# Performance work log

Measured on AMD Instinct MI355X. Metric: run time of the kernel, lower is better.

## Reference

```python
import jax, jax.numpy as jnp
import numpy as np

GRID_SIZE = 5
SPLINE_ORDER = 3
NUM_BASIS = GRID_SIZE + SPLINE_ORDER  # 8


def make_grid():
    # knots: grid_size + 2*spline_order + 1 = 12 points over extended [-1,1]
    h = 2.0 / GRID_SIZE
    return (jnp.arange(-SPLINE_ORDER, GRID_SIZE + SPLINE_ORDER + 1, dtype=jnp.float32) * h - 1.0)[None, :]  # (1, 12)


def b_splines(x, grid):
    # x: (N, in) -> bases: (N, in, NUM_BASIS) via Cox-de Boor recursion
    x = x[..., None]  # (N, in, 1)
    bases = ((x >= grid[:, :-1]) & (x < grid[:, 1:])).astype(x.dtype)
    for p in range(1, SPLINE_ORDER + 1):
        left = (x - grid[:, : -(p + 1)]) / (grid[:, p:-1] - grid[:, : -(p + 1)])
        right = (grid[:, p + 1:] - x) / (grid[:, p + 1:] - grid[:, 1:-p])
        bases = left * bases[..., :-1] + right * bases[..., 1:]
    return bases


def kan_linear(x, base_w, spline_w, scaler, grid):
    # x: (N, in); base_w: (out, in); spline_w: (out, in, G); scaler: (out, in)
    base = jnp.einsum('ni,oi->no', jax.nn.silu(x), base_w)
    bases = b_splines(x, grid)  # (N, in, G)
    spline = jnp.einsum('nig,oig->no', bases, spline_w * scaler[..., None])
    return base + spline


def setup_inputs() -> dict:
    key = jax.random.key(0)
    ks = jax.random.split(key, 7)
    H, L = 768, 2
    hidden = jax.random.normal(ks[0], (32, 512, H), dtype=jnp.float32)
    s = 0.1
    return {
        'hidden': hidden,
        'base_w1': jax.random.normal(ks[1], (H, H), jnp.float32) * s,
        'spline_w1': jax.random.normal(ks[2], (H, H, NUM_BASIS), jnp.float32) * s,
        'scaler1': jax.random.normal(ks[3], (H, H), jnp.float32) * s + 1.0,
        'base_w2': jax.random.normal(ks[4], (L, H), jnp.float32) * s,
        'spline_w2': jax.random.normal(ks[5], (L, H, NUM_BASIS), jnp.float32) * s,
        'scaler2': jax.random.normal(ks[6], (L, H), jnp.float32) * s + 1.0,
    }


def reference(hidden, base_w1, spline_w1, scaler1, base_w2, spline_w2, scaler2):
    grid = make_grid()
    B, S, H = hidden.shape
    x = hidden.reshape(-1, H)  # (N, H)
    x = kan_linear(x, base_w1, spline_w1, scaler1, grid)
    x = jax.nn.gelu(x, approximate=False)  # torch F.gelu default = erf
    out = kan_linear(x, base_w2, spline_w2, scaler2, grid)  # (N, L)
    return out.reshape(B, S, -1).squeeze(-1) if out.shape[-1] == 1 else out.reshape(B, S, -1)
```

## Files before the change

### kernel.cpp

```cpp
#include <hip/hip_runtime.h>
#include <math.h>

#define NROWS 16384
#define H     768
#define KEXP  6912
#define NCHUNK 108
#define NITER 54

typedef __attribute__((ext_vector_type(8))) short  bhalf8;
typedef __attribute__((ext_vector_type(4))) float  floatx4;

__device__ __forceinline__ unsigned short f2bf(float f) {
    unsigned int u = __float_as_uint(f);
    u = (u + 0x7FFFu + ((u >> 16) & 1u)) >> 16;
    return (unsigned short)u;
}
__device__ __forceinline__ float bf2f(unsigned short h) {
    return __uint_as_float(((unsigned int)h) << 16);
}
__device__ __forceinline__ unsigned int pack2(unsigned short a, unsigned short b) {
    return (unsigned int)a | ((unsigned int)b << 16);
}
__device__ __forceinline__ float silu_f(float x) { return x / (1.0f + __expf(-x)); }

__device__ __forceinline__ float gelu_fast(float x) {
    float x3 = x * x * x;
    float y = fmaf(x3, 0.0356774081f, x * 0.7978845608f);
    float e = __expf(2.0f * y);
    float th = 1.0f - 2.0f / (e + 1.0f);
    return 0.5f * x * (1.0f + th);
}

__device__ __forceinline__ void kan_bases(float x, float* __restrict__ b) {
    const float c6 = 0.166666666667f;
    float u  = fmaf(x, 2.5f, 5.5f);
    float fj = floorf(u);
    float t  = u - fj;
    int  j0  = (int)fj;
    float t2 = t * t, t3 = t2 * t;
    float n0 = t3 * c6;
    float n1 = fmaf(t3, -0.5f, fmaf(t2, 0.5f, fmaf(t, 0.5f, c6)));
    float n2 = fmaf(t3, 0.5f, fmaf(t2, -1.0f, 0.666666666667f));
    float omt = 1.0f - t;
    float n3 = omt * omt * omt * c6;
#pragma unroll
    for (int c = 0; c < 8; ++c) {
        int d = j0 - c;
        float v = (d == 0) ? n0 : 0.0f;
        v = (d == 1) ? n1 : v;
        v = (d == 2) ? n2 : v;
        v = (d == 3) ? n3 : v;
        b[c] = v;
    }
}

__global__ __launch_bounds__(256) void prep_expand(
    const float* __restrict__ x, const float* __restrict__ bw,
    const float* __restrict__ sw, const float* __restrict__ sc,
    unsigned short* __restrict__ wp, unsigned short* __restrict__ F)
{
    const int b = blockIdx.x, t = threadIdx.x;
    if (b < 6144) {
        const int e0 = b * 2048 + t;
#pragma unroll
        for (int j = 0; j < 8; ++j) {
            int e = e0 + j * 256;
            int n = e / 768;
            int i = e - n * 768;
            float xv = x[e];
            unsigned short* out = F + (size_t)n * KEXP;
            out[i] = f2bf(silu_f(xv));
            float bb[8];
            kan_bases(xv, bb);
            uint4 pk;
            pk.x = pack2(f2bf(bb[0]), f2bf(bb[1]));
            pk.y = pack2(f2bf(bb[2]), f2bf(bb[3]));
            pk.z = pack2(f2bf(bb[4]), f2bf(bb[5]));
            pk.w = pack2(f2bf(bb[6]), f2bf(bb[7]));
            *(uint4*)(out + H + (size_t)i * 8) = pk;
        }
    } else {
        const int n = b - 6144;
        const float* bwr = bw + (size_t)n * H;
        unsigned short* out = wp + (size_t)n * KEXP;
        if (t < 96) {
            const float4* xp = (const float4*)(bwr + t * 8);
            float4 v0 = xp[0], v1 = xp[1];
            uint4 pk;
            pk.x = pack2(f2bf(v0.x), f2bf(v0.y));
            pk.y = pack2(f2bf(v0.z), f2bf(v0.w));
            pk.z = pack2(f2bf(v1.x), f2bf(v1.y));
            pk.w = pack2(f2bf(v1.z), f2bf(v1.w));
            *(uint4*)(out + t * 8) = pk;
        }
#pragma unroll
        for (int p = 0; p < 3; ++p) {
            int i = t + p * 256;
            float s = sc[(size_t)n * H + i];
            const float4* swp = (const float4*)(sw + ((size_t)n * H + i) * 8);
            float4 w0 = swp[0], w1 = swp[1];
            uint4 pk;
            pk.x = pack2(f2bf(w0.x * s), f2bf(w0.y * s));
            pk.y = pack2(f2bf(w0.z * s), f2bf(w0.w * s));
            pk.z = pack2(f2bf(w1.x * s), f2bf(w1.y * s));
            pk.w = pack2(f2bf(w1.z * s), f2bf(w1.w * s));
            *(uint4*)(out + H + (size_t)i * 8) = pk;
        }
    }
}


#define AS1 __attribute__((address_space(1)))
#define AS3 __attribute__((address_space(3)))

#define DSR(D, A, O) asm volatile("ds_read_b128 %0, %1 offset:" #O : "=v"(D) : "v"(A) : "memory")
#define LDA0(O) do{ DSR(fA0[0],avA[0],O); DSR(fA0[1],avA[1],O); DSR(fA0[2],avA[2],O); DSR(fA0[3],avA[3],O); \
                    DSR(fA0[4],avA[4],O); DSR(fA0[5],avA[5],O); DSR(fA0[6],avA[6],O); DSR(fA0[7],avA[7],O); }while(0)
#define LDA1(O) do{ DSR(fA1[0],avA[0],O); DSR(fA1[1],avA[1],O); DSR(fA1[2],avA[2],O); DSR(fA1[3],avA[3],O); \
                    DSR(fA1[4],avA[4],O); DSR(fA1[5],avA[5],O); DSR(fA1[6],avA[6],O); DSR(fA1[7],avA[7],O); }while(0)
#define LDB(O)  do{ DSR(fB[0],avB[0],O); DSR(fB[1],avB[1],O); }while(0)

#define MM0(QN) do{ \
    _Pragma("unroll") \
    for (int kk = 0; kk < 2; ++kk) \
        _Pragma("unroll") \
        for (int im = 0; im < 4; ++im) \
            acc0[QN][im] = __builtin_amdgcn_mfma_f32_16x16x32_bf16( \
                fA0[im*2+kk], fB[kk], acc0[QN][im], 0, 0, 0); \
}while(0)
#define MM1(QN) do{ \
    _Pragma("unroll") \
    for (int kk = 0; kk < 2; ++kk) \
        _Pragma("unroll") \
        for (int im = 0; im < 4; ++im) \
            acc1[QN][im] = __builtin_amdgcn_mfma_f32_16x16x32_bf16( \
                fA1[im*2+kk], fB[kk], acc1[QN][im], 0, 0, 0); \
}while(0)

#define STG_A(BF,HH,KS) do{ \
    __builtin_amdgcn_global_load_lds((const AS1 void*)(pA##HH[0] + (size_t)(KS)*64), \
        (AS3 void*)&sA[BF][HH][wb8], 16, 0, 0); \
    __builtin_amdgcn_global_load_lds((const AS1 void*)(pA##HH[1] + (size_t)(KS)*64), \
        (AS3 void*)&sA[BF][HH][4096 + wb8], 16, 0, 0); \
}while(0)
#define STG_B(BF,QN,KS) \
    __builtin_amdgcn_global_load_lds((const AS1 void*)(pB[QN] + (size_t)(KS)*64), \
        (AS3 void*)&sB[BF][QN][wb8], 16, 0, 0)

#define PH_MID do{ __builtin_amdgcn_s_barrier(); \
    asm volatile("s_waitcnt lgkmcnt(0)" ::: "memory"); \
    __builtin_amdgcn_sched_barrier(0); \
    __builtin_amdgcn_s_setprio(1); }while(0)
#define PH_END do{ __builtin_amdgcn_s_setprio(0); \
    __builtin_amdgcn_sched_barrier(0); \
    __builtin_amdgcn_s_barrier(); }while(0)
#define PH_END_VMN(N) do{ __builtin_amdgcn_s_setprio(0); \
    __builtin_amdgcn_sched_barrier(0); \
    asm volatile("s_waitcnt vmcnt(" #N ")" ::: "memory"); \
    __builtin_amdgcn_s_barrier(); }while(0)

#define EPI_HALF(ACC, QMOFF) do{ \
    _Pragma("unroll") \
    for (int im = 0; im < 4; ++im) { \
        _Pragma("unroll") \
        for (int rg = 0; rg < 4; ++rg) { \
            float p0 = 0.f, p1 = 0.f; \
            _Pragma("unroll") \
            for (int qn = 0; qn < 3; ++qn) { \
                float v = ACC[qn][im][rg]; \
                float u = gelu_fast(v); \
                float f0v = silu_f(u); \
                float bb[8]; \
                kan_bases(u, bb); \
                float t0 = bb[0]*wsw[qn][0][0].x + bb[1]*wsw[qn][0][0].y \
                         + bb[2]*wsw[qn][0][0].z + bb[3]*wsw[qn][0][0].w \
                         + bb[4]*wsw[qn][0][1].x + bb[5]*wsw[qn][0][1].y \
                         + bb[6]*wsw[qn][0][1].z + bb[7]*wsw[qn][0][1].w; \
                float t1 = bb[0]*wsw[qn][1][0].x + bb[1]*wsw[qn][1][0].y \
                         + bb[2]*wsw[qn][1][0].z + bb[3]*wsw[qn][1][0].w \
                         + bb[4]*wsw[qn][1][1].x + bb[5]*wsw[qn][1][1].y \
                         + bb[6]*wsw[qn][1][1].z + bb[7]*wsw[qn][1][1].w; \
                p0 += fmaf(f0v, wbw[qn][0], wsc[qn][0] * t0); \
                p1 += fmaf(f0v, wbw[qn][1], wsc[qn][1] * t1); \
            } \
            _Pragma("unroll") \
            for (int off = 8; off > 0; off >>= 1) { \
                p0 += __shfl_xor(p0, off, 64); \
                p1 += __shfl_xor(p1, off, 64); \
            } \
            if (lm == 0) { \
                int row = rowBase + (QMOFF) + wr*64 + im*16 + quad*4 + rg; \
                atomicAdd(&outp[(size_t)row * 2 + 0], p0); \
                atomicAdd(&outp[(size_t)row * 2 + 1], p1); \
            } \
        } \
    } \
}while(0)

__global__ __launch_bounds__(512, 2) void kan1_fused(
    const unsigned short* __restrict__ F, const unsigned short* __restrict__ wp,
    const float* __restrict__ bw2, const float* __restrict__ sw2,
    const float* __restrict__ sc2, float* __restrict__ outp)
{
    __shared__ __align__(16) unsigned short sA[2][2][8192];
    __shared__ __align__(16) unsigned short sB[2][3][4096];

    const int b = blockIdx.x;
    const int s = b >> 3;
    const int rowT = (b & 7) * 8 + (s >> 2);
    const int colT = s & 3;
    const int rowBase = rowT * 256, colBase = colT * 192;

    const int t = threadIdx.x;
    const int lane = t & 63;
    const int quad = lane >> 4, lm = lane & 15, p7 = lane & 7;
    const int wv = t >> 6, wr = wv & 1, wc = wv >> 1;

    const int rr = t >> 3;
    const int slotx = (t & 7) ^ (rr & 7);
    const int wb8 = (t & 448) * 8;

    const unsigned short* pA0[2]; const unsigned short* pA1[2];
    const unsigned short* pB[3];
#pragma unroll
    for (int p = 0; p < 2; ++p) {
        pA0[p] = F + (size_t)(rowBase +       p*64 + rr) * KEXP + slotx*8;
        pA1[p] = F + (size_t)(rowBase + 128 + p*64 + rr) * KEXP + slotx*8;
    }
#pragma unroll
    for (int q = 0; q < 3; ++q)
        pB[q] = wp + (size_t)(colBase + q*64 + rr) * KEXP + slotx*8;

    unsigned int avA[8], avB[2];
    {
        unsigned int aB = (unsigned int)(size_t)(AS3 unsigned short*)&sA[0][0][0];
        unsigned int bB = (unsigned int)(size_t)(AS3 unsigned short*)&sB[0][0][0];
#pragma unroll
        for (int im = 0; im < 4; ++im)
#pragma unroll
            for (int kk = 0; kk < 2; ++kk)
                avA[im*2+kk] = aB + (unsigned)(((wr*64 + im*16 + lm)*64 + (((kk*4+quad)^p7)*8)) * 2);
#pragma unroll
        for (int kk = 0; kk < 2; ++kk)
            avB[kk] = bB + (unsigned)(((wc*16 + lm)*64 + (((kk*4+quad)^p7)*8)) * 2);
    }

    floatx4 acc0[3][4] = {};
    floatx4 acc1[3][4] = {};
    bhalf8 fA0[8], fA1[8], fB[2];

    STG_A(0,0,0); STG_A(0,1,0); STG_B(0,0,0); STG_B(0,1,0); STG_B(0,2,0);
    STG_A(1,0,1); STG_A(1,1,1); STG_B(1,0,1); STG_B(1,1,1);
    asm volatile("s_waitcnt vmcnt(8)" ::: "memory");
    __builtin_amdgcn_s_barrier();

#pragma unroll 1
    for (int i = 0; i < NITER; ++i) {
        const int k1 = 2*i + 1;
        const int k2 = (2*i + 2 > 107) ? 107 : 2*i + 2;
        const int k3 = (2*i + 3 > 107) ? 107 : 2*i + 3;
        LDA0(0);     LDB(0);     STG_B(1,2,k1);               PH_MID; MM0(0);         PH_END_VMN(10);
        LDA1(16384);             STG_A(0,0,k2);               PH_MID; MM1(0);         PH_END_VMN(10);
        LDB(8192);               STG_A(0,1,k2);               PH_MID; MM1(1); MM0(1); PH_END_VMN(11);
        LDB(16384);              STG_B(0,0,k2); STG_B(0,1,k2);PH_MID; MM0(2); MM1(2); PH_END_VMN(8);
        LDA0(32768); LDB(24576); STG_B(0,2,k2);               PH_MID; MM0(0);         PH_END;
        LDA1(49152);             STG_A(1,0,k3);               PH_MID; MM1(0);         PH_END_VMN(10);
        LDB(32768);              STG_A(1,1,k3);               PH_MID; MM1(1); MM0(1); PH_END_VMN(11);
        LDB(40960);              STG_B(1,0,k3); STG_B(1,1,k3);PH_MID; MM0(2); MM1(2); PH_END_VMN(8);
    }

    float  wbw[3][2], wsc[3][2];
    float4 wsw[3][2][2];
#pragma unroll
    for (int qn = 0; qn < 3; ++qn) {
        const int i = colBase + qn*64 + wc*16 + lm;
        wbw[qn][0] = bw2[i];      wbw[qn][1] = bw2[H + i];
        wsc[qn][0] = sc2[i];      wsc[qn][1] = sc2[H + i];
        const float4* q0 = (const float4*)(sw2 + (size_t)i * 8);
        const float4* q1 = (const float4*)(sw2 + (size_t)(H + i) * 8);
        wsw[qn][0][0] = q0[0];    wsw[qn][0][1] = q0[1];
        wsw[qn][1][0] = q1[0];    wsw[qn][1][1] = q1[1];
    }
    EPI_HALF(acc0, 0);
    EPI_HALF(acc1, 128);
}

extern "C" void kernel_launch(void* const* d_in, const int* in_sizes, int n_in,
                              void* d_out, int out_size, void* d_ws, size_t ws_size,
                              hipStream_t stream) {
    const float* hidden = (const float*)d_in[0];
    const float* bw1    = (const float*)d_in[1];
    const float* sw1    = (const float*)d_in[2];
    const float* sc1    = (const float*)d_in[3];
    const float* bw2    = (const float*)d_in[4];
    const float* sw2    = (const float*)d_in[5];
    const float* sc2    = (const float*)d_in[6];
    float* out = (float*)d_out;

    const size_t wp_elems = (size_t)H * KEXP;
    unsigned short* wp = (unsigned short*)d_ws;
    unsigned short* F  = wp + wp_elems;

    hipMemsetAsync(d_out, 0, (size_t)out_size, stream);
    prep_expand<<<6144 + H, 256, 0, stream>>>(hidden, bw1, sw1, sc1, wp, F);
    kan1_fused<<<256, 512, 0, stream>>>(F, wp, bw2, sw2, sc2, out);
}
```

Measured before the change: 324.6 us.

## Use fast reciprocals, nontemporal stores, restructure epilogue loops, relax launch bounds

Swaps the divisions in silu and gelu for hardware reciprocal approximations, and makes the prep kernel's expanded-feature and weight writes nontemporal. The epilogue loop order changes so each column tile's second-layer weights are loaded just before use instead of being held in registers for the whole kernel, with per-row partial sums accumulated across column tiles. Launch bounds go from 2 blocks per CU to 1, which gives the compiler more registers but may lower occupancy. The reciprocal approximation slightly reduces accuracy.

```diff
diff --git a/kernel.cpp b/kernel.cpp
--- a/kernel.cpp
+++ b/kernel.cpp
@@ -9,6 +9,7 @@
 
 typedef __attribute__((ext_vector_type(8))) short  bhalf8;
 typedef __attribute__((ext_vector_type(4))) float  floatx4;
+typedef __attribute__((ext_vector_type(4))) unsigned int uintx4;
 
 __device__ __forceinline__ unsigned short f2bf(float f) {
     unsigned int u = __float_as_uint(f);
@@ -21,13 +22,15 @@
 __device__ __forceinline__ unsigned int pack2(unsigned short a, unsigned short b) {
     return (unsigned int)a | ((unsigned int)b << 16);
 }
-__device__ __forceinline__ float silu_f(float x) { return x / (1.0f + __expf(-x)); }
+__device__ __forceinline__ float silu_f(float x) {
+    return x * __builtin_amdgcn_rcpf(1.0f + __expf(-x));
+}
 
 __device__ __forceinline__ float gelu_fast(float x) {
     float x3 = x * x * x;
     float y = fmaf(x3, 0.0356774081f, x * 0.7978845608f);
     float e = __expf(2.0f * y);
-    float th = 1.0f - 2.0f / (e + 1.0f);
+    float th = 1.0f - 2.0f * __builtin_amdgcn_rcpf(e + 1.0f);
     return 0.5f * x * (1.0f + th);
 }
 
@@ -69,15 +72,15 @@
             int i = e - n * 768;
             float xv = x[e];
             unsigned short* out = F + (size_t)n * KEXP;
-            out[i] = f2bf(silu_f(xv));
+            __builtin_nontemporal_store(f2bf(silu_f(xv)), out + i);
             float bb[8];
             kan_bases(xv, bb);
-            uint4 pk;
+            uintx4 pk;
             pk.x = pack2(f2bf(bb[0]), f2bf(bb[1]));
             pk.y = pack2(f2bf(bb[2]), f2bf(bb[3]));
             pk.z = pack2(f2bf(bb[4]), f2bf(bb[5]));
             pk.w = pack2(f2bf(bb[6]), f2bf(bb[7]));
-            *(uint4*)(out + H + (size_t)i * 8) = pk;
+            __builtin_nontemporal_store(pk, (uintx4*)(out + H + (size_t)i * 8));
         }
     } else {
         const int n = b - 6144;
@@ -86,12 +89,12 @@
         if (t < 96) {
             const float4* xp = (const float4*)(bwr + t * 8);
             float4 v0 = xp[0], v1 = xp[1];
-            uint4 pk;
+            uintx4 pk;
             pk.x = pack2(f2bf(v0.x), f2bf(v0.y));
             pk.y = pack2(f2bf(v0.z), f2bf(v0.w));
             pk.z = pack2(f2bf(v1.x), f2bf(v1.y));
             pk.w = pack2(f2bf(v1.z), f2bf(v1.w));
-            *(uint4*)(out + t * 8) = pk;
+            __builtin_nontemporal_store(pk, (uintx4*)(out + t * 8));
         }
 #pragma unroll
         for (int p = 0; p < 3; ++p) {
@@ -99,12 +102,12 @@
             float s = sc[(size_t)n * H + i];
             const float4* swp = (const float4*)(sw + ((size_t)n * H + i) * 8);
             float4 w0 = swp[0], w1 = swp[1];
-            uint4 pk;
+            uintx4 pk;
             pk.x = pack2(f2bf(w0.x * s), f2bf(w0.y * s));
             pk.y = pack2(f2bf(w0.z * s), f2bf(w0.w * s));
             pk.z = pack2(f2bf(w1.x * s), f2bf(w1.y * s));
             pk.w = pack2(f2bf(w1.z * s), f2bf(w1.w * s));
-            *(uint4*)(out + H + (size_t)i * 8) = pk;
+            __builtin_nontemporal_store(pk, (uintx4*)(out + H + (size_t)i * 8));
         }
     }
 }
@@ -160,44 +163,51 @@
     __builtin_amdgcn_s_barrier(); }while(0)
 
 #define EPI_HALF(ACC, QMOFF) do{ \
-    _Pragma("unroll") \
-    for (int im = 0; im < 4; ++im) { \
+    float pa[4][4] = {}, pb[4][4] = {}; \
+    _Pragma("unroll") \
+    for (int qn = 0; qn < 3; ++qn) { \
+        const int i = colBase + qn*64 + wc*16 + lm; \
+        const float bwa = bw2[i], bwb = bw2[H + i]; \
+        const float sca = sc2[i], scb = sc2[H + i]; \
+        const float4* q0 = (const float4*)(sw2 + (size_t)i * 8); \
+        const float4* q1 = (const float4*)(sw2 + (size_t)(H + i) * 8); \
+        const float4 wa0 = q0[0], wa1 = q0[1]; \
+        const float4 wb0 = q1[0], wb1 = q1[1]; \
+        _Pragma("unroll") \
+        for (int im = 0; im < 4; ++im) \
         _Pragma("unroll") \
         for (int rg = 0; rg < 4; ++rg) { \
-            float p0 = 0.f, p1 = 0.f; \
-            _Pragma("unroll") \
-            for (int qn = 0; qn < 3; ++qn) { \
-                float v = ACC[qn][im][rg]; \
-                float u = gelu_fast(v); \
-                float f0v = silu_f(u); \
-                float bb[8]; \
-                kan_bases(u, bb); \
-                float t0 = bb[0]*wsw[qn][0][0].x + bb[1]*wsw[qn][0][0].y \
-                         + bb[2]*wsw[qn][0][0].z + bb[3]*wsw[qn][0][0].w \
-                         + bb[4]*wsw[qn][0][1].x + bb[5]*wsw[qn][0][1].y \
-                         + bb[6]*wsw[qn][0][1].z + bb[7]*wsw[qn][0][1].w; \
-                float t1 = bb[0]*wsw[qn][1][0].x + bb[1]*wsw[qn][1][0].y \
-                         + bb[2]*wsw[qn][1][0].z + bb[3]*wsw[qn][1][0].w \
-                         + bb[4]*wsw[qn][1][1].x + bb[5]*wsw[qn][1][1].y \
-                         + bb[6]*wsw[qn][1][1].z + bb[7]*wsw[qn][1][1].w; \
-                p0 += fmaf(f0v, wbw[qn][0], wsc[qn][0] * t0); \
-                p1 += fmaf(f0v, wbw[qn][1], wsc[qn][1] * t1); \
-            } \
-            _Pragma("unroll") \
-            for (int off = 8; off > 0; off >>= 1) { \
-                p0 += __shfl_xor(p0, off, 64); \
-                p1 += __shfl_xor(p1, off, 64); \
-            } \
-            if (lm == 0) { \
-                int row = rowBase + (QMOFF) + wr*64 + im*16 + quad*4 + rg; \
-                atomicAdd(&outp[(size_t)row * 2 + 0], p0); \
-                atomicAdd(&outp[(size_t)row * 2 + 1], p1); \
-            } \
+            float u = gelu_fast(ACC[qn][im][rg]); \
+            float f0v = silu_f(u); \
+            float bb[8]; \
+            kan_bases(u, bb); \
+            float t0 = bb[0]*wa0.x + bb[1]*wa0.y + bb[2]*wa0.z + bb[3]*wa0.w \
+                     + bb[4]*wa1.x + bb[5]*wa1.y + bb[6]*wa1.z + bb[7]*wa1.w; \
+            float t1 = bb[0]*wb0.x + bb[1]*wb0.y + bb[2]*wb0.z + bb[3]*wb0.w \
+                     + bb[4]*wb1.x + bb[5]*wb1.y + bb[6]*wb1.z + bb[7]*wb1.w; \
+            pa[im][rg] += fmaf(f0v, bwa, sca * t0); \
+            pb[im][rg] += fmaf(f0v, bwb, scb * t1); \
+        } \
+    } \
+    _Pragma("unroll") \
+    for (int im = 0; im < 4; ++im) \
+    _Pragma("unroll") \
+    for (int rg = 0; rg < 4; ++rg) { \
+        float a0 = pa[im][rg], a1 = pb[im][rg]; \
+        _Pragma("unroll") \
+        for (int off = 8; off > 0; off >>= 1) { \
+            a0 += __shfl_xor(a0, off, 64); \
+            a1 += __shfl_xor(a1, off, 64); \
+        } \
+        if (lm == 0) { \
+            const int row = rowBase + (QMOFF) + wr*64 + im*16 + quad*4 + rg; \
+            atomicAdd(&outp[(size_t)row * 2 + 0], a0); \
+            atomicAdd(&outp[(size_t)row * 2 + 1], a1); \
         } \
     } \
 }while(0)
 
-__global__ __launch_bounds__(512, 2) void kan1_fused(
+__global__ __launch_bounds__(512, 1) void kan1_fused(
     const unsigned short* __restrict__ F, const unsigned short* __restrict__ wp,
     const float* __restrict__ bw2, const float* __restrict__ sw2,
     const float* __restrict__ sc2, float* __restrict__ outp)
@@ -269,18 +279,6 @@
         LDB(40960);              STG_B(1,0,k3); STG_B(1,1,k3);PH_MID; MM0(2); MM1(2); PH_END_VMN(8);
     }
 
-    float  wbw[3][2], wsc[3][2];
-    float4 wsw[3][2][2];
-#pragma unroll
-    for (int qn = 0; qn < 3; ++qn) {
-        const int i = colBase + qn*64 + wc*16 + lm;
-        wbw[qn][0] = bw2[i];      wbw[qn][1] = bw2[H + i];
-        wsc[qn][0] = sc2[i];      wsc[qn][1] = sc2[H + i];
-        const float4* q0 = (const float4*)(sw2 + (size_t)i * 8);
-        const float4* q1 = (const float4*)(sw2 + (size_t)(H + i) * 8);
-        wsw[qn][0][0] = q0[0];    wsw[qn][0][1] = q0[1];
-        wsw[qn][1][0] = q1[0];    wsw[qn][1][1] = q1[1];
-    }
     EPI_HALF(acc0, 0);
     EPI_HALF(acc1, 128);
 }
```

Result: faster. 310.8 us, median of 2 (-4.3%).
